# Kernel tuning notes

Measured on AMD Instinct MI355X. Metric: run time of the kernel, lower is better.

Reference implementation:

```python
import jax, jax.numpy as jnp
import numpy as np

WSZ = 8
DIM = 256
DIM_HEAD = 32
HEADS = DIM // DIM_HEAD
INNER = HEADS * DIM_HEAD
D4 = DIM // 4
SCALE = DIM_HEAD ** -0.5
EPS = 1e-5


def _rel_pos_tables():
    s = WSZ
    pos = np.stack(np.meshgrid(np.arange(s), np.arange(s), indexing='ij'), 0).reshape(2, -1).T  # (s*s, 2)
    rel = pos[:, None] - pos[None, :]
    rel[..., 0] += s - 1
    rel[..., 1] += s - 1
    idx = rel[..., 0] * (2 * s - 1) + rel[..., 1]  # (s*s, s*s)
    grid = np.stack(np.meshgrid(np.arange(-s, s + 1), np.arange(-s, s + 1), indexing='ij'), 0).reshape(2, -1).T
    return idx.astype(np.int32), grid.astype(np.float32)  # ((2s+1)^2, 2)

_REL_IDX_NP, _REL_GRID_NP = _rel_pos_tables()


def _ln(h, gamma, beta):
    m = h.mean(-1, keepdims=True)
    v = ((h - m) ** 2).mean(-1, keepdims=True)
    return (h - m) / jnp.sqrt(v + EPS) * gamma + beta


def setup_inputs() -> dict:
    key = jax.random.key(0)
    ks = jax.random.split(key, 8)
    p = {}
    p['x'] = jax.random.normal(ks[0], (4, DIM, 256, 256), jnp.float32)
    p['g'] = jnp.ones((DIM,), jnp.float32)
    p['b'] = jnp.zeros((DIM,), jnp.float32)
    p['w_qkv'] = jax.random.normal(ks[1], (3 * INNER, DIM), jnp.float32) * 0.02
    p['w_out'] = jax.random.normal(ks[2], (DIM, INNER), jnp.float32) * 0.02
    p['b_out'] = jnp.zeros((DIM,), jnp.float32)
    p['dpb_w1'] = jax.random.normal(ks[3], (2, D4), jnp.float32) * 0.02
    p['dpb_b1'] = jnp.zeros((D4,), jnp.float32)
    p['dpb_ln1_g'] = jnp.ones((D4,), jnp.float32)
    p['dpb_ln1_b'] = jnp.zeros((D4,), jnp.float32)
    p['dpb_w2'] = jax.random.normal(ks[4], (D4, D4), jnp.float32) * 0.02
    p['dpb_b2'] = jnp.zeros((D4,), jnp.float32)
    p['dpb_ln2_g'] = jnp.ones((D4,), jnp.float32)
    p['dpb_ln2_b'] = jnp.zeros((D4,), jnp.float32)
    p['dpb_w3'] = jax.random.normal(ks[5], (D4, D4), jnp.float32) * 0.02
    p['dpb_b3'] = jnp.zeros((D4,), jnp.float32)
    p['dpb_ln3_g'] = jnp.ones((D4,), jnp.float32)
    p['dpb_ln3_b'] = jnp.zeros((D4,), jnp.float32)
    p['dpb_w4'] = jax.random.normal(ks[6], (D4, 1), jnp.float32) * 0.02
    p['dpb_b4'] = jnp.zeros((1,), jnp.float32)
    return p


def reference(x, g, b, w_qkv, w_out, b_out,
              dpb_w1, dpb_b1, dpb_ln1_g, dpb_ln1_b,
              dpb_w2, dpb_b2, dpb_ln2_g, dpb_ln2_b,
              dpb_w3, dpb_b3, dpb_ln3_g, dpb_ln3_b,
              dpb_w4, dpb_b4):
    B, D, H, W = x.shape
    s = WSZ
    nH, nW = H // s, W // s
    ss = s * s

    # channel-first LayerNorm over dim axis (biased var)
    mean = x.mean(1, keepdims=True)
    var = ((x - mean) ** 2).mean(1, keepdims=True)
    xn = (x - mean) / jnp.sqrt(var + EPS) * g[None, :, None, None] + b[None, :, None, None]

    # short attention: non-overlapping windows -> (B*nH*nW, D, s, s)
    xw = xn.reshape(B, D, nH, s, nW, s).transpose(0, 2, 4, 1, 3, 5).reshape(-1, D, s, s)
    nb = xw.shape[0]

    # 1x1 conv qkv projection (no bias)
    qkv = jnp.einsum('ed,bdxy->bexy', w_qkv, xw)  # (nb, 3*INNER, s, s)
    q, k, v = jnp.split(qkv, 3, axis=1)
    def to_heads(t):  # (nb, INNER, s, s) -> (nb, heads, ss, dh)
        return t.reshape(nb, HEADS, DIM_HEAD, ss).transpose(0, 1, 3, 2)
    q, k, v = to_heads(q) * SCALE, to_heads(k), to_heads(v)

    sim = jnp.einsum('bhid,bhjd->bhij', q, k)  # (nb, heads, ss, ss)

    # dynamic position bias MLP over ((2s+1)^2, 2) relative coords
    rel = jnp.asarray(_REL_GRID_NP)
    h1 = jax.nn.relu(_ln(rel @ dpb_w1 + dpb_b1, dpb_ln1_g, dpb_ln1_b))
    h2 = jax.nn.relu(_ln(h1 @ dpb_w2 + dpb_b2, dpb_ln2_g, dpb_ln2_b))
    h3 = jax.nn.relu(_ln(h2 @ dpb_w3 + dpb_b3, dpb_ln3_g, dpb_ln3_b))
    table = (h3 @ dpb_w4 + dpb_b4)[:, 0]  # ((2s+1)^2,)
    bias = table[jnp.asarray(_REL_IDX_NP)]  # (ss, ss)

    attn = jax.nn.softmax(sim + bias, axis=-1)
    out = jnp.einsum('bhij,bhjd->bhid', attn, v)  # (nb, heads, ss, dh)
    out = out.transpose(0, 1, 3, 2).reshape(nb, INNER, s, s)

    # 1x1 conv output projection (with bias)
    out = jnp.einsum('od,bdxy->boxy', w_out, out) + b_out[None, :, None, None]

    # un-window
    out = out.reshape(B, nH, nW, D, s, s).transpose(0, 3, 1, 4, 2, 5).reshape(B, D, H, W)
    return out
```

## Files before the change

### kernel.cpp

```cpp
#include <hip/hip_runtime.h>

typedef __attribute__((ext_vector_type(8))) short short8;
typedef __attribute__((ext_vector_type(4))) float f32x4;

#define SCALE_Q 0.17677669529663687f

__device__ __forceinline__ unsigned short f2bf(float f){
  unsigned u = __builtin_bit_cast(unsigned, f);
  u = (u + 0x7FFFu + ((u >> 16) & 1u)) >> 16;
  return (unsigned short)u;
}
__device__ __forceinline__ float bf2f(unsigned short h){
  unsigned u = ((unsigned)h) << 16;
  return __builtin_bit_cast(float, u);
}

__global__ void prep_w(const float* __restrict__ w_qkv, const float* __restrict__ g,
                       const float* __restrict__ bvec, const float* __restrict__ w_out,
                       unsigned short* __restrict__ wq_b, unsigned short* __restrict__ wo_b,
                       float* __restrict__ qkvb){
  const int row  = blockIdx.x * 4 + (threadIdx.x >> 6);
  const int lane = threadIdx.x & 63;
  if (row < 768){
    const float sc = (row < 256) ? SCALE_Q : 1.0f;
    float4 w  = ((const float4*)(w_qkv + (size_t)row * 256))[lane];
    float4 gv = ((const float4*)g)[lane];
    float4 bv = ((const float4*)bvec)[lane];
    unsigned long long pk =
        (unsigned long long)f2bf(w.x * gv.x * sc)
      | ((unsigned long long)f2bf(w.y * gv.y * sc) << 16)
      | ((unsigned long long)f2bf(w.z * gv.z * sc) << 32)
      | ((unsigned long long)f2bf(w.w * gv.w * sc) << 48);
    *(unsigned long long*)(wq_b + (size_t)row * 256 + lane * 4) = pk;
    float acc = w.x * bv.x + w.y * bv.y + w.z * bv.z + w.w * bv.w;
    #pragma unroll
    for (int off = 32; off; off >>= 1) acc += __shfl_xor(acc, off);
    if (lane == 0) qkvb[row] = acc * sc;
  } else {
    const int o = row - 768;
    float4 w = ((const float4*)(w_out + (size_t)o * 256))[lane];
    unsigned long long pk =
        (unsigned long long)f2bf(w.x)
      | ((unsigned long long)f2bf(w.y) << 16)
      | ((unsigned long long)f2bf(w.z) << 32)
      | ((unsigned long long)f2bf(w.w) << 48);
    *(unsigned long long*)(wo_b + (size_t)o * 256 + lane * 4) = pk;
  }
}

__device__ __forceinline__ float wsum(float v){
  #pragma unroll
  for (int off = 32; off; off >>= 1) v += __shfl_xor(v, off);
  return v;
}
__device__ __forceinline__ float lnrelu(float h, float gamma, float beta){
  float m = wsum(h) * (1.0f / 64.0f);
  float d = h - m;
  float v = wsum(d * d) * (1.0f / 64.0f);
  float r = d * rsqrtf(v + 1e-5f) * gamma + beta;
  return fmaxf(r, 0.0f);
}
__device__ __forceinline__ float matmul64(float h, const float* __restrict__ w, int f){
  float acc = 0.0f;
  for (int k = 0; k < 64; ++k) acc += __shfl(h, k) * w[k * 64 + f];
  return acc;
}

__global__ void dpb_kernel(const float* __restrict__ w1, const float* __restrict__ b1,
                           const float* __restrict__ g1, const float* __restrict__ e1,
                           const float* __restrict__ w2, const float* __restrict__ b2,
                           const float* __restrict__ g2, const float* __restrict__ e2,
                           const float* __restrict__ w3, const float* __restrict__ b3,
                           const float* __restrict__ g3, const float* __restrict__ e3,
                           const float* __restrict__ w4, const float* __restrict__ b4,
                           float* __restrict__ table){
  const int r = blockIdx.x, f = threadIdx.x;
  const float cy = (float)(r / 17 - 8), cx = (float)(r % 17 - 8);
  float h = cy * w1[f] + cx * w1[64 + f] + b1[f];
  h = lnrelu(h, g1[f], e1[f]);
  float h2 = matmul64(h, w2, f) + b2[f];
  h2 = lnrelu(h2, g2[f], e2[f]);
  float h3 = matmul64(h2, w3, f) + b3[f];
  h3 = lnrelu(h3, g3[f], e3[f]);
  float o = wsum(h3 * w4[f]);
  if (f == 0) table[r] = o + b4[0];
}

__global__ void bias_expand(const float* __restrict__ table, float* __restrict__ bias64){
  const int id = blockIdx.x * 256 + threadIdx.x;
  const int i = id >> 6, j = id & 63;
  const int r0 = (i >> 3) - (j >> 3) + 7;
  const int r1 = (i & 7) - (j & 7) + 7;
  bias64[id] = table[r0 * 15 + r1];
}

#define LDS_TOTAL 148480

__global__ __launch_bounds__(256, 1) void attn_main(
    const float* __restrict__ x,
    const unsigned short* __restrict__ wq_b,
    const unsigned short* __restrict__ wo_b,
    const float* __restrict__ qkvb,
    const float* __restrict__ b_out,
    const float* __restrict__ bias64,
    float* __restrict__ out)
{
  extern __shared__ char smem[];
  unsigned short* xn = (unsigned short*)smem;
  unsigned short* Qs = (unsigned short*)(smem + 36864);
  unsigned short* Ks = (unsigned short*)(smem + 70656);
  unsigned short* Vt = (unsigned short*)(smem + 104448);

  const int tid = threadIdx.x, lane = tid & 63, wv = tid >> 6;
  const int blk = ((blockIdx.x & 7) << 9) | (blockIdx.x >> 3);
  const int b = blk >> 10, hb = (blk >> 5) & 31, wb = blk & 31;

  {
    const int p = lane, prow = p >> 3, pcol = p & 7;
    const float* xp = x + ((size_t)b << 24) + (size_t)(hb * 8 + prow) * 256 + (size_t)(wb * 8 + pcol);
    float sum = 0.0f, ss = 0.0f;
    unsigned short* xrow = xn + p * 264;
    #pragma unroll 8
    for (int dk = 0; dk < 64; ++dk){
      const int d = (wv << 6) + dk;
      float v = xp[(size_t)d << 16];
      sum += v; ss += v * v;
      xrow[d] = f2bf(v);
    }
    float* red = (float*)(smem + 141312);
    red[wv * 64 + p] = sum;
    red[256 + wv * 64 + p] = ss;
    __syncthreads();
    float s0 = red[p] + red[64 + p] + red[128 + p] + red[192 + p];
    float s1 = red[256 + p] + red[320 + p] + red[384 + p] + red[448 + p];
    float mean = s0 * (1.0f / 256.0f);
    float var  = s1 * (1.0f / 256.0f) - mean * mean;
    float rstd = rsqrtf(var + 1e-5f);
    if (wv == 0){ red[512 + p] = mean; red[576 + p] = rstd; }
    __syncthreads();
    const int pp = tid >> 2, qq = tid & 3;
    const float mn = red[512 + pp], rs = red[576 + pp];
    unsigned short* rowp = xn + pp * 264 + qq * 64;
    #pragma unroll
    for (int i = 0; i < 8; ++i){
      short8 v8 = *(short8*)(rowp + i * 8);
      #pragma unroll
      for (int e = 0; e < 8; ++e){
        float f = bf2f((unsigned short)v8[e]);
        v8[e] = (short)f2bf((f - mn) * rs);
      }
      *(short8*)(rowp + i * 8) = v8;
    }
  }
  __syncthreads();

  {
    const int l15 = lane & 15, l4 = lane >> 4;
    for (int c = 0; c < 3; ++c){
      const int n0 = wv * 192 + c * 64;
      f32x4 acc[4][4];
      #pragma unroll
      for (int mt = 0; mt < 4; ++mt)
        #pragma unroll
        for (int nt = 0; nt < 4; ++nt)
          acc[mt][nt] = (f32x4){0.f, 0.f, 0.f, 0.f};
      const unsigned short* bp = wq_b + (size_t)(n0 + l15) * 256 + 8 * l4;
      short8 bcur[4], bnxt[4];
      #pragma unroll
      for (int nt = 0; nt < 4; ++nt) bcur[nt] = *(const short8*)(bp + nt * 4096);
      #pragma unroll
      for (int kt = 0; kt < 8; ++kt){
        if (kt < 7){
          #pragma unroll
          for (int nt = 0; nt < 4; ++nt) bnxt[nt] = *(const short8*)(bp + nt * 4096 + (kt + 1) * 32);
        }
        short8 a[4];
        #pragma unroll
        for (int mt = 0; mt < 4; ++mt)
          a[mt] = *(const short8*)(xn + (mt * 16 + l15) * 264 + kt * 32 + 8 * l4);
        #pragma unroll
        for (int mt = 0; mt < 4; ++mt)
          #pragma unroll
          for (int nt = 0; nt < 4; ++nt)
            acc[mt][nt] = __builtin_amdgcn_mfma_f32_16x16x32_bf16(a[mt], bcur[nt], acc[mt][nt], 0, 0, 0);
        if (kt < 7){
          #pragma unroll
          for (int nt = 0; nt < 4; ++nt) bcur[nt] = bnxt[nt];
        }
      }
      const bool isV = (n0 >= 512);
      const bool isQ = (n0 < 256);
      #pragma unroll
      for (int nt = 0; nt < 4; ++nt){
        const int e = n0 + nt * 16 + l15;
        const float bv = qkvb[e];
        #pragma unroll
        for (int mt = 0; mt < 4; ++mt){
          if (!isV){
            unsigned short* dst = isQ ? Qs : Ks;
            const int col = e & 255;
            #pragma unroll
            for (int j = 0; j < 4; ++j){
              const int row = mt * 16 + (l4 << 2) + j;
              dst[row * 264 + col] = f2bf(acc[mt][nt][j] + bv);
            }
          } else {
            const int vd = e - 512;
            const int r0 = mt * 16 + (l4 << 2);
            unsigned long long pk =
                (unsigned long long)f2bf(acc[mt][nt][0] + bv)
              | ((unsigned long long)f2bf(acc[mt][nt][1] + bv) << 16)
              | ((unsigned long long)f2bf(acc[mt][nt][2] + bv) << 32)
              | ((unsigned long long)f2bf(acc[mt][nt][3] + bv) << 48);
            *(unsigned long long*)(Vt + vd * 72 + r0) = pk;
          }
        }
      }
    }
  }
  __syncthreads();

  {
    const int l15 = lane & 15, l4 = lane >> 4;
    unsigned short* Pw = ((unsigned short*)smem) + wv * 4608;
    f32x4 oacc[2][4][2];
    #pragma unroll
    for (int hh = 0; hh < 2; ++hh){
      const int h = (wv << 1) + hh;
      short8 qa[4], kb[4];
      #pragma unroll
      for (int t = 0; t < 4; ++t){
        qa[t] = *(const short8*)(Qs + (t * 16 + l15) * 264 + h * 32 + 8 * l4);
        kb[t] = *(const short8*)(Ks + (t * 16 + l15) * 264 + h * 32 + 8 * l4);
      }
      #pragma unroll
      for (int mt = 0; mt < 4; ++mt){
        f32x4 srow[4];
        #pragma unroll
        for (int nt = 0; nt < 4; ++nt){
          f32x4 z = {0.f, 0.f, 0.f, 0.f};
          srow[nt] = __builtin_amdgcn_mfma_f32_16x16x32_bf16(qa[mt], kb[nt], z, 0, 0, 0);
        }
        #pragma unroll
        for (int j = 0; j < 4; ++j){
          const int row = mt * 16 + (l4 << 2) + j;
          float v0 = srow[0][j] + bias64[row * 64 +      l15];
          float v1 = srow[1][j] + bias64[row * 64 + 16 + l15];
          float v2 = srow[2][j] + bias64[row * 64 + 32 + l15];
          float v3 = srow[3][j] + bias64[row * 64 + 48 + l15];
          float m = fmaxf(fmaxf(v0, v1), fmaxf(v2, v3));
          m = fmaxf(m, __shfl_xor(m, 1)); m = fmaxf(m, __shfl_xor(m, 2));
          m = fmaxf(m, __shfl_xor(m, 4)); m = fmaxf(m, __shfl_xor(m, 8));
          v0 = __expf(v0 - m); v1 = __expf(v1 - m);
          v2 = __expf(v2 - m); v3 = __expf(v3 - m);
          float sm = v0 + v1 + v2 + v3;
          sm += __shfl_xor(sm, 1); sm += __shfl_xor(sm, 2);
          sm += __shfl_xor(sm, 4); sm += __shfl_xor(sm, 8);
          const float inv = 1.0f / sm;
          Pw[row * 72 +      l15] = f2bf(v0 * inv);
          Pw[row * 72 + 16 + l15] = f2bf(v1 * inv);
          Pw[row * 72 + 32 + l15] = f2bf(v2 * inv);
          Pw[row * 72 + 48 + l15] = f2bf(v3 * inv);
        }
      }
      #pragma unroll
      for (int mt = 0; mt < 4; ++mt)
        #pragma unroll
        for (int nt = 0; nt < 2; ++nt)
          oacc[hh][mt][nt] = (f32x4){0.f, 0.f, 0.f, 0.f};
      #pragma unroll
      for (int kt = 0; kt < 2; ++kt){
        short8 pa[4], vb[2];
        #pragma unroll
        for (int mt = 0; mt < 4; ++mt)
          pa[mt] = *(const short8*)(Pw + (mt * 16 + l15) * 72 + kt * 32 + 8 * l4);
        #pragma unroll
        for (int nt = 0; nt < 2; ++nt)
          vb[nt] = *(const short8*)(Vt + (h * 32 + nt * 16 + l15) * 72 + kt * 32 + 8 * l4);
        #pragma unroll
        for (int mt = 0; mt < 4; ++mt)
          #pragma unroll
          for (int nt = 0; nt < 2; ++nt)
            oacc[hh][mt][nt] = __builtin_amdgcn_mfma_f32_16x16x32_bf16(pa[mt], vb[nt], oacc[hh][mt][nt], 0, 0, 0);
      }
    }
    __syncthreads();
    unsigned short* ao = (unsigned short*)smem;
    #pragma unroll
    for (int hh = 0; hh < 2; ++hh){
      const int h = (wv << 1) + hh;
      #pragma unroll
      for (int mt = 0; mt < 4; ++mt)
        #pragma unroll
        for (int nt = 0; nt < 2; ++nt)
          #pragma unroll
          for (int j = 0; j < 4; ++j)
            ao[(mt * 16 + (l4 << 2) + j) * 264 + h * 32 + nt * 16 + l15] = f2bf(oacc[hh][mt][nt][j]);
    }
  }
  __syncthreads();

  {
    const int l15 = lane & 15, l4 = lane >> 4;
    const unsigned short* ao = (const unsigned short*)smem;
    float* sw = (float*)(smem + 143872) + wv * 288;
    const int n0w = wv * 64;
    f32x4 acc[4][4];
    #pragma unroll
    for (int mt = 0; mt < 4; ++mt)
      #pragma unroll
      for (int nt = 0; nt < 4; ++nt)
        acc[mt][nt] = (f32x4){0.f, 0.f, 0.f, 0.f};
    const unsigned short* bp = wo_b + (size_t)(n0w + l15) * 256 + 8 * l4;
    short8 bcur[4], bnxt[4];
    #pragma unroll
    for (int nt = 0; nt < 4; ++nt) bcur[nt] = *(const short8*)(bp + nt * 4096);
    #pragma unroll
    for (int kt = 0; kt < 8; ++kt){
      if (kt < 7){
        #pragma unroll
        for (int nt = 0; nt < 4; ++nt) bnxt[nt] = *(const short8*)(bp + nt * 4096 + (kt + 1) * 32);
      }
      short8 a[4];
      #pragma unroll
      for (int mt = 0; mt < 4; ++mt)
        a[mt] = *(const short8*)(ao + (mt * 16 + l15) * 264 + kt * 32 + 8 * l4);
      #pragma unroll
      for (int mt = 0; mt < 4; ++mt)
        #pragma unroll
        for (int nt = 0; nt < 4; ++nt)
          acc[mt][nt] = __builtin_amdgcn_mfma_f32_16x16x32_bf16(a[mt], bcur[nt], acc[mt][nt], 0, 0, 0);
      if (kt < 7){
        #pragma unroll
        for (int nt = 0; nt < 4; ++nt) bcur[nt] = bnxt[nt];
      }
    }
    float* op = out + ((size_t)b << 24) + (size_t)(hb * 8) * 256 + (size_t)(wb * 8);
    #pragma unroll
    for (int nt = 0; nt < 4; ++nt){
      const int ebase = n0w + nt * 16;
      const float bo = b_out[ebase + l15];
      #pragma unroll
      for (int mt = 0; mt < 4; ++mt){
        #pragma unroll
        for (int j = 0; j < 4; ++j)
          sw[((l4 << 2) + j) * 17 + l15] = acc[mt][nt][j] + bo;
        asm volatile("s_waitcnt lgkmcnt(0)" ::: "memory");
        #pragma unroll
        for (int q = 0; q < 4; ++q){
          const int el = q * 4 + l4;
          float v = sw[l15 * 17 + el];
          const int p = mt * 16 + l15;
          op[(size_t)(ebase + el) * 65536 + (size_t)(p >> 3) * 256 + (p & 7)] = v;
        }
        asm volatile("s_waitcnt lgkmcnt(0)" ::: "memory");
      }
    }
  }
}

extern "C" void kernel_launch(void* const* d_in, const int* in_sizes, int n_in,
                              void* d_out, int out_size, void* d_ws, size_t ws_size,
                              hipStream_t stream){
  const float* x     = (const float*)d_in[0];
  const float* g     = (const float*)d_in[1];
  const float* bvec  = (const float*)d_in[2];
  const float* w_qkv = (const float*)d_in[3];
  const float* w_out = (const float*)d_in[4];
  const float* b_out = (const float*)d_in[5];
  float* out = (float*)d_out;

  char* ws = (char*)d_ws;
  unsigned short* wq_b  = (unsigned short*)(ws);
  unsigned short* wo_b  = (unsigned short*)(ws + 393216);
  float* qkvb   = (float*)(ws + 524288);
  float* table  = (float*)(ws + 527360);
  float* bias64 = (float*)(ws + 528640);

  prep_w<<<dim3(256), dim3(256), 0, stream>>>(w_qkv, g, bvec, w_out, wq_b, wo_b, qkvb);
  dpb_kernel<<<dim3(289), dim3(64), 0, stream>>>(
      (const float*)d_in[6],  (const float*)d_in[7],  (const float*)d_in[8],  (const float*)d_in[9],
      (const float*)d_in[10], (const float*)d_in[11], (const float*)d_in[12], (const float*)d_in[13],
      (const float*)d_in[14], (const float*)d_in[15], (const float*)d_in[16], (const float*)d_in[17],
      (const float*)d_in[18], (const float*)d_in[19], table);
  bias_expand<<<dim3(16), dim3(256), 0, stream>>>(table, bias64);

  hipFuncSetAttribute((const void*)attn_main, hipFuncAttributeMaxDynamicSharedMemorySize, LDS_TOTAL);
  attn_main<<<dim3(4096), dim3(256), LDS_TOTAL, stream>>>(x, wq_b, wo_b, qkvb, b_out, bias64, out);
}
```

Before: 1.075 ms.

## Use 1024-thread blocks with pre-tiled MFMA weights and swizzled P buffer

The main attention kernel goes from 4 to 16 waves per block. Each wave now takes a smaller slice of the QKV GEMM, one head-half of the attention, and a 32x32 tile of the output projection. The weights are pre-arranged into the MFMA fragment layout, so each lane does one contiguous 16-byte load. The softmax probability buffer uses an XOR swizzle to cut LDS bank conflicts. The aim is more latency hiding inside each CU, since only one block fits per CU because of LDS. The cost is fewer MFMAs per wave to amortise loads over, plus extra barriers.

```diff
diff --git a/kernel.cpp b/kernel.cpp
--- a/kernel.cpp
+++ b/kernel.cpp
@@ -15,37 +15,42 @@
   return __builtin_bit_cast(float, u);
 }
 
-__global__ void prep_w(const float* __restrict__ w_qkv, const float* __restrict__ g,
-                       const float* __restrict__ bvec, const float* __restrict__ w_out,
-                       unsigned short* __restrict__ wq_b, unsigned short* __restrict__ wo_b,
-                       float* __restrict__ qkvb){
-  const int row  = blockIdx.x * 4 + (threadIdx.x >> 6);
+__global__ void prep_tiled(const float* __restrict__ w_qkv, const float* __restrict__ g,
+                           const float* __restrict__ w_out,
+                           unsigned short* __restrict__ wq_t, unsigned short* __restrict__ wo_t){
+  int id = blockIdx.x * 256 + threadIdx.x;
+  const bool isQKV = (id < 24576);
+  int e, sub;
+  const float* src;
+  unsigned short* dst;
+  float sc;
+  if (isQKV){ e = id >> 5; sub = id & 31; src = w_qkv; dst = wq_t; sc = (e < 256) ? SCALE_Q : 1.0f; }
+  else { int id2 = id - 24576; e = id2 >> 5; sub = id2 & 31; src = w_out; dst = wo_t; sc = 1.0f; }
+  const int kt = sub >> 2, l4c = sub & 3;
+  const int k0 = kt * 32 + l4c * 8;
+  const int tile = e >> 4, l15c = e & 15;
+  const float4 w0 = *(const float4*)(src + (size_t)e * 256 + k0);
+  const float4 w1 = *(const float4*)(src + (size_t)e * 256 + k0 + 4);
+  float4 g0 = make_float4(1.f,1.f,1.f,1.f), g1 = g0;
+  if (isQKV){ g0 = *(const float4*)(g + k0); g1 = *(const float4*)(g + k0 + 4); }
+  short8 o;
+  o[0] = (short)f2bf(w0.x * g0.x * sc); o[1] = (short)f2bf(w0.y * g0.y * sc);
+  o[2] = (short)f2bf(w0.z * g0.z * sc); o[3] = (short)f2bf(w0.w * g0.w * sc);
+  o[4] = (short)f2bf(w1.x * g1.x * sc); o[5] = (short)f2bf(w1.y * g1.y * sc);
+  o[6] = (short)f2bf(w1.z * g1.z * sc); o[7] = (short)f2bf(w1.w * g1.w * sc);
+  *(short8*)(dst + ((size_t)(tile * 8 + kt) * 64 + (l4c * 16 + l15c)) * 8) = o;
+}
+
+__global__ void qkvb_kernel(const float* __restrict__ w_qkv, const float* __restrict__ bvec,
+                            float* __restrict__ qkvb){
+  const int row = blockIdx.x * 4 + (threadIdx.x >> 6);
   const int lane = threadIdx.x & 63;
-  if (row < 768){
-    const float sc = (row < 256) ? SCALE_Q : 1.0f;
-    float4 w  = ((const float4*)(w_qkv + (size_t)row * 256))[lane];
-    float4 gv = ((const float4*)g)[lane];
-    float4 bv = ((const float4*)bvec)[lane];
-    unsigned long long pk =
-        (unsigned long long)f2bf(w.x * gv.x * sc)
-      | ((unsigned long long)f2bf(w.y * gv.y * sc) << 16)
-      | ((unsigned long long)f2bf(w.z * gv.z * sc) << 32)
-      | ((unsigned long long)f2bf(w.w * gv.w * sc) << 48);
-    *(unsigned long long*)(wq_b + (size_t)row * 256 + lane * 4) = pk;
-    float acc = w.x * bv.x + w.y * bv.y + w.z * bv.z + w.w * bv.w;
-    #pragma unroll
-    for (int off = 32; off; off >>= 1) acc += __shfl_xor(acc, off);
-    if (lane == 0) qkvb[row] = acc * sc;
-  } else {
-    const int o = row - 768;
-    float4 w = ((const float4*)(w_out + (size_t)o * 256))[lane];
-    unsigned long long pk =
-        (unsigned long long)f2bf(w.x)
-      | ((unsigned long long)f2bf(w.y) << 16)
-      | ((unsigned long long)f2bf(w.z) << 32)
-      | ((unsigned long long)f2bf(w.w) << 48);
-    *(unsigned long long*)(wo_b + (size_t)o * 256 + lane * 4) = pk;
-  }
+  float4 w  = ((const float4*)(w_qkv + (size_t)row * 256))[lane];
+  float4 bv = ((const float4*)bvec)[lane];
+  float acc = w.x * bv.x + w.y * bv.y + w.z * bv.z + w.w * bv.w;
+  #pragma unroll
+  for (int off = 32; off; off >>= 1) acc += __shfl_xor(acc, off);
+  if (lane == 0) qkvb[row] = acc * ((row < 256) ? SCALE_Q : 1.0f);
 }
 
 __device__ __forceinline__ float wsum(float v){
@@ -94,12 +99,16 @@
   bias64[id] = table[r0 * 15 + r1];
 }
 
-#define LDS_TOTAL 148480
-
-__global__ __launch_bounds__(256, 1) void attn_main(
+#define LDS_TOTAL 146944
+
+__device__ __forceinline__ int pswz(int row, int col){
+  return row * 64 + (((col >> 3) ^ (row & 7)) << 3) + (col & 7);
+}
+
+__global__ __launch_bounds__(1024, 1) void attn_main(
     const float* __restrict__ x,
-    const unsigned short* __restrict__ wq_b,
-    const unsigned short* __restrict__ wo_b,
+    const unsigned short* __restrict__ wq_t,
+    const unsigned short* __restrict__ wo_t,
     const float* __restrict__ qkvb,
     const float* __restrict__ b_out,
     const float* __restrict__ bias64,
@@ -107,11 +116,13 @@
 {
   extern __shared__ char smem[];
   unsigned short* xn = (unsigned short*)smem;
-  unsigned short* Qs = (unsigned short*)(smem + 36864);
-  unsigned short* Ks = (unsigned short*)(smem + 70656);
-  unsigned short* Vt = (unsigned short*)(smem + 104448);
+  unsigned short* Qs = (unsigned short*)(smem + 33792);
+  unsigned short* Ks = (unsigned short*)(smem + 67584);
+  unsigned short* Vt = (unsigned short*)(smem + 101376);
+  float* red = (float*)(smem + 138240);
 
   const int tid = threadIdx.x, lane = tid & 63, wv = tid >> 6;
+  const int l15 = lane & 15, l4 = lane >> 4;
   const int blk = ((blockIdx.x & 7) << 9) | (blockIdx.x >> 3);
   const int b = blk >> 10, hb = (blk >> 5) & 31, wb = blk & 31;
 
@@ -120,29 +131,31 @@
     const float* xp = x + ((size_t)b << 24) + (size_t)(hb * 8 + prow) * 256 + (size_t)(wb * 8 + pcol);
     float sum = 0.0f, ss = 0.0f;
     unsigned short* xrow = xn + p * 264;
-    #pragma unroll 8
-    for (int dk = 0; dk < 64; ++dk){
-      const int d = (wv << 6) + dk;
+    #pragma unroll
+    for (int i = 0; i < 16; ++i){
+      const int d = (wv << 4) + i;
       float v = xp[(size_t)d << 16];
       sum += v; ss += v * v;
       xrow[d] = f2bf(v);
     }
-    float* red = (float*)(smem + 141312);
     red[wv * 64 + p] = sum;
-    red[256 + wv * 64 + p] = ss;
+    red[1024 + wv * 64 + p] = ss;
     __syncthreads();
-    float s0 = red[p] + red[64 + p] + red[128 + p] + red[192 + p];
-    float s1 = red[256 + p] + red[320 + p] + red[384 + p] + red[448 + p];
-    float mean = s0 * (1.0f / 256.0f);
-    float var  = s1 * (1.0f / 256.0f) - mean * mean;
-    float rstd = rsqrtf(var + 1e-5f);
-    if (wv == 0){ red[512 + p] = mean; red[576 + p] = rstd; }
+    if (wv == 0){
+      float s0 = 0.f, s1 = 0.f;
+      #pragma unroll
+      for (int w = 0; w < 16; ++w){ s0 += red[w * 64 + lane]; s1 += red[1024 + w * 64 + lane]; }
+      float mean = s0 * (1.0f / 256.0f);
+      float var  = s1 * (1.0f / 256.0f) - mean * mean;
+      red[2048 + lane] = mean;
+      red[2112 + lane] = rsqrtf(var + 1e-5f);
+    }
     __syncthreads();
-    const int pp = tid >> 2, qq = tid & 3;
-    const float mn = red[512 + pp], rs = red[576 + pp];
-    unsigned short* rowp = xn + pp * 264 + qq * 64;
-    #pragma unroll
-    for (int i = 0; i < 8; ++i){
+    const int pp = tid >> 4, qq = tid & 15;
+    const float mn = red[2048 + pp], rs = red[2112 + pp];
+    unsigned short* rowp = xn + pp * 264 + qq * 16;
+    #pragma unroll
+    for (int i = 0; i < 2; ++i){
       short8 v8 = *(short8*)(rowp + i * 8);
       #pragma unroll
       for (int e = 0; e < 8; ++e){
@@ -155,65 +168,48 @@
   __syncthreads();
 
   {
-    const int l15 = lane & 15, l4 = lane >> 4;
-    for (int c = 0; c < 3; ++c){
-      const int n0 = wv * 192 + c * 64;
-      f32x4 acc[4][4];
-      #pragma unroll
-      for (int mt = 0; mt < 4; ++mt)
-        #pragma unroll
-        for (int nt = 0; nt < 4; ++nt)
-          acc[mt][nt] = (f32x4){0.f, 0.f, 0.f, 0.f};
-      const unsigned short* bp = wq_b + (size_t)(n0 + l15) * 256 + 8 * l4;
-      short8 bcur[4], bnxt[4];
-      #pragma unroll
-      for (int nt = 0; nt < 4; ++nt) bcur[nt] = *(const short8*)(bp + nt * 4096);
-      #pragma unroll
-      for (int kt = 0; kt < 8; ++kt){
-        if (kt < 7){
+    const int wm = wv >> 3, wn = wv & 7;
+    f32x4 acc[2][6];
+    #pragma unroll
+    for (int mt = 0; mt < 2; ++mt)
+      #pragma unroll
+      for (int nt = 0; nt < 6; ++nt)
+        acc[mt][nt] = (f32x4){0.f, 0.f, 0.f, 0.f};
+    #pragma unroll
+    for (int kt = 0; kt < 8; ++kt){
+      short8 a0 = *(const short8*)(xn + (wm * 32 +      l15) * 264 + kt * 32 + l4 * 8);
+      short8 a1 = *(const short8*)(xn + (wm * 32 + 16 + l15) * 264 + kt * 32 + l4 * 8);
+      const unsigned short* wp = wq_t + ((size_t)(wn * 6 * 8 + kt) * 64 + lane) * 8;
+      short8 bb[6];
+      #pragma unroll
+      for (int nt = 0; nt < 6; ++nt) bb[nt] = *(const short8*)(wp + (size_t)nt * 4096);
+      #pragma unroll
+      for (int nt = 0; nt < 6; ++nt){
+        acc[0][nt] = __builtin_amdgcn_mfma_f32_16x16x32_bf16(a0, bb[nt], acc[0][nt], 0, 0, 0);
+        acc[1][nt] = __builtin_amdgcn_mfma_f32_16x16x32_bf16(a1, bb[nt], acc[1][nt], 0, 0, 0);
+      }
+    }
+    #pragma unroll
+    for (int nt = 0; nt < 6; ++nt){
+      const int e = wn * 96 + nt * 16 + l15;
+      const float bv = qkvb[e];
+      #pragma unroll
+      for (int mt = 0; mt < 2; ++mt){
+        const int r0 = wm * 32 + mt * 16 + (l4 << 2);
+        if (e < 512){
+          unsigned short* dst = (e < 256) ? Qs : Ks;
+          const int col = e & 255;
           #pragma unroll
-          for (int nt = 0; nt < 4; ++nt) bnxt[nt] = *(const short8*)(bp + nt * 4096 + (kt + 1) * 32);
-        }
-        short8 a[4];
-        #pragma unroll
-        for (int mt = 0; mt < 4; ++mt)
-          a[mt] = *(const short8*)(xn + (mt * 16 + l15) * 264 + kt * 32 + 8 * l4);
-        #pragma unroll
-        for (int mt = 0; mt < 4; ++mt)
-          #pragma unroll
-          for (int nt = 0; nt < 4; ++nt)
-            acc[mt][nt] = __builtin_amdgcn_mfma_f32_16x16x32_bf16(a[mt], bcur[nt], acc[mt][nt], 0, 0, 0);
-        if (kt < 7){
-          #pragma unroll
-          for (int nt = 0; nt < 4; ++nt) bcur[nt] = bnxt[nt];
-        }
-      }
-      const bool isV = (n0 >= 512);
-      const bool isQ = (n0 < 256);
-      #pragma unroll
-      for (int nt = 0; nt < 4; ++nt){
-        const int e = n0 + nt * 16 + l15;
-        const float bv = qkvb[e];
-        #pragma unroll
-        for (int mt = 0; mt < 4; ++mt){
-          if (!isV){
-            unsigned short* dst = isQ ? Qs : Ks;
-            const int col = e & 255;
-            #pragma unroll
-            for (int j = 0; j < 4; ++j){
-              const int row = mt * 16 + (l4 << 2) + j;
-              dst[row * 264 + col] = f2bf(acc[mt][nt][j] + bv);
-            }
-          } else {
-            const int vd = e - 512;
-            const int r0 = mt * 16 + (l4 << 2);
-            unsigned long long pk =
-                (unsigned long long)f2bf(acc[mt][nt][0] + bv)
-              | ((unsigned long long)f2bf(acc[mt][nt][1] + bv) << 16)
-              | ((unsigned long long)f2bf(acc[mt][nt][2] + bv) << 32)
-              | ((unsigned long long)f2bf(acc[mt][nt][3] + bv) << 48);
-            *(unsigned long long*)(Vt + vd * 72 + r0) = pk;
-          }
+          for (int j = 0; j < 4; ++j)
+            dst[(r0 + j) * 264 + col] = f2bf(acc[mt][nt][j] + bv);
+        } else {
+          const int vd = e - 512;
+          unsigned long long pk =
+              (unsigned long long)f2bf(acc[mt][nt][0] + bv)
+            | ((unsigned long long)f2bf(acc[mt][nt][1] + bv) << 16)
+            | ((unsigned long long)f2bf(acc[mt][nt][2] + bv) << 32)
+            | ((unsigned long long)f2bf(acc[mt][nt][3] + bv) << 48);
+          *(unsigned long long*)(Vt + vd * 72 + r0) = pk;
         }
       }
     }
@@ -221,136 +217,120 @@
   __syncthreads();
 
   {
-    const int l15 = lane & 15, l4 = lane >> 4;
-    unsigned short* Pw = ((unsigned short*)smem) + wv * 4608;
-    f32x4 oacc[2][4][2];
-    #pragma unroll
-    for (int hh = 0; hh < 2; ++hh){
-      const int h = (wv << 1) + hh;
-      short8 qa[4], kb[4];
-      #pragma unroll
-      for (int t = 0; t < 4; ++t){
-        qa[t] = *(const short8*)(Qs + (t * 16 + l15) * 264 + h * 32 + 8 * l4);
-        kb[t] = *(const short8*)(Ks + (t * 16 + l15) * 264 + h * 32 + 8 * l4);
-      }
-      #pragma unroll
-      for (int mt = 0; mt < 4; ++mt){
-        f32x4 srow[4];
-        #pragma unroll
-        for (int nt = 0; nt < 4; ++nt){
-          f32x4 z = {0.f, 0.f, 0.f, 0.f};
-          srow[nt] = __builtin_amdgcn_mfma_f32_16x16x32_bf16(qa[mt], kb[nt], z, 0, 0, 0);
-        }
-        #pragma unroll
-        for (int j = 0; j < 4; ++j){
-          const int row = mt * 16 + (l4 << 2) + j;
-          float v0 = srow[0][j] + bias64[row * 64 +      l15];
-          float v1 = srow[1][j] + bias64[row * 64 + 16 + l15];
-          float v2 = srow[2][j] + bias64[row * 64 + 32 + l15];
-          float v3 = srow[3][j] + bias64[row * 64 + 48 + l15];
-          float m = fmaxf(fmaxf(v0, v1), fmaxf(v2, v3));
-          m = fmaxf(m, __shfl_xor(m, 1)); m = fmaxf(m, __shfl_xor(m, 2));
-          m = fmaxf(m, __shfl_xor(m, 4)); m = fmaxf(m, __shfl_xor(m, 8));
-          v0 = __expf(v0 - m); v1 = __expf(v1 - m);
-          v2 = __expf(v2 - m); v3 = __expf(v3 - m);
-          float sm = v0 + v1 + v2 + v3;
-          sm += __shfl_xor(sm, 1); sm += __shfl_xor(sm, 2);
-          sm += __shfl_xor(sm, 4); sm += __shfl_xor(sm, 8);
-          const float inv = 1.0f / sm;
-          Pw[row * 72 +      l15] = f2bf(v0 * inv);
-          Pw[row * 72 + 16 + l15] = f2bf(v1 * inv);
-          Pw[row * 72 + 32 + l15] = f2bf(v2 * inv);
-          Pw[row * 72 + 48 + l15] = f2bf(v3 * inv);
-        }
-      }
-      #pragma unroll
-      for (int mt = 0; mt < 4; ++mt)
+    const int h = wv >> 1, half = wv & 1;
+    short8 qa[2], kb[4];
+    #pragma unroll
+    for (int mt = 0; mt < 2; ++mt)
+      qa[mt] = *(const short8*)(Qs + (half * 32 + mt * 16 + l15) * 264 + h * 32 + l4 * 8);
+    #pragma unroll
+    for (int t = 0; t < 4; ++t)
+      kb[t] = *(const short8*)(Ks + (t * 16 + l15) * 264 + h * 32 + l4 * 8);
+    __syncthreads();
+
+    unsigned short* Pw = (unsigned short*)smem + h * 4096;
+    #pragma unroll
+    for (int mt = 0; mt < 2; ++mt){
+      f32x4 srow[4];
+      #pragma unroll
+      for (int nt = 0; nt < 4; ++nt){
+        f32x4 z = {0.f, 0.f, 0.f, 0.f};
+        srow[nt] = __builtin_amdgcn_mfma_f32_16x16x32_bf16(qa[mt], kb[nt], z, 0, 0, 0);
+      }
+      #pragma unroll
+      for (int j = 0; j < 4; ++j){
+        const int row = half * 32 + mt * 16 + (l4 << 2) + j;
+        float v0 = srow[0][j] + bias64[row * 64 +      l15];
+        float v1 = srow[1][j] + bias64[row * 64 + 16 + l15];
+        float v2 = srow[2][j] + bias64[row * 64 + 32 + l15];
+        float v3 = srow[3][j] + bias64[row * 64 + 48 + l15];
+        float m = fmaxf(fmaxf(v0, v1), fmaxf(v2, v3));
+        m = fmaxf(m, __shfl_xor(m, 1)); m = fmaxf(m, __shfl_xor(m, 2));
+        m = fmaxf(m, __shfl_xor(m, 4)); m = fmaxf(m, __shfl_xor(m, 8));
+        v0 = __expf(v0 - m); v1 = __expf(v1 - m);
+        v2 = __expf(v2 - m); v3 = __expf(v3 - m);
+        float sm = v0 + v1 + v2 + v3;
+        sm += __shfl_xor(sm, 1); sm += __shfl_xor(sm, 2);
+        sm += __shfl_xor(sm, 4); sm += __shfl_xor(sm, 8);
+        const float inv = 1.0f / sm;
+        Pw[pswz(row,      l15)] = f2bf(v0 * inv);
+        Pw[pswz(row, 16 + l15)] = f2bf(v1 * inv);
+        Pw[pswz(row, 32 + l15)] = f2bf(v2 * inv);
+        Pw[pswz(row, 48 + l15)] = f2bf(v3 * inv);
+      }
+    }
+    f32x4 oacc[2][2];
+    #pragma unroll
+    for (int mt = 0; mt < 2; ++mt)
+      #pragma unroll
+      for (int nt = 0; nt < 2; ++nt)
+        oacc[mt][nt] = (f32x4){0.f, 0.f, 0.f, 0.f};
+    #pragma unroll
+    for (int ktv = 0; ktv < 2; ++ktv){
+      short8 pa[2], vb[2];
+      #pragma unroll
+      for (int mt = 0; mt < 2; ++mt){
+        const int row = half * 32 + mt * 16 + l15;
+        pa[mt] = *(const short8*)(Pw + row * 64 + (((ktv * 4 + l4) ^ (row & 7)) << 3));
+      }
+      #pragma unroll
+      for (int nt = 0; nt < 2; ++nt)
+        vb[nt] = *(const short8*)(Vt + (h * 32 + nt * 16 + l15) * 72 + ktv * 32 + l4 * 8);
+      #pragma unroll
+      for (int mt = 0; mt < 2; ++mt)
         #pragma unroll
         for (int nt = 0; nt < 2; ++nt)
-          oacc[hh][mt][nt] = (f32x4){0.f, 0.f, 0.f, 0.f};
-      #pragma unroll
-      for (int kt = 0; kt < 2; ++kt){
-        short8 pa[4], vb[2];
-        #pragma unroll
-        for (int mt = 0; mt < 4; ++mt)
-          pa[mt] = *(const short8*)(Pw + (mt * 16 + l15) * 72 + kt * 32 + 8 * l4);
-        #pragma unroll
-        for (int nt = 0; nt < 2; ++nt)
-          vb[nt] = *(const short8*)(Vt + (h * 32 + nt * 16 + l15) * 72 + kt * 32 + 8 * l4);
-        #pragma unroll
-        for (int mt = 0; mt < 4; ++mt)
-          #pragma unroll
-          for (int nt = 0; nt < 2; ++nt)
-            oacc[hh][mt][nt] = __builtin_amdgcn_mfma_f32_16x16x32_bf16(pa[mt], vb[nt], oacc[hh][mt][nt], 0, 0, 0);
-      }
+          oacc[mt][nt] = __builtin_amdgcn_mfma_f32_16x16x32_bf16(pa[mt], vb[nt], oacc[mt][nt], 0, 0, 0);
     }
     __syncthreads();
     unsigned short* ao = (unsigned short*)smem;
     #pragma unroll
-    for (int hh = 0; hh < 2; ++hh){
-      const int h = (wv << 1) + hh;
-      #pragma unroll
-      for (int mt = 0; mt < 4; ++mt)
+    for (int mt = 0; mt < 2; ++mt)
+      #pragma unroll
+      for (int nt = 0; nt < 2; ++nt)
         #pragma unroll
-        for (int nt = 0; nt < 2; ++nt)
-          #pragma unroll
-          for (int j = 0; j < 4; ++j)
-            ao[(mt * 16 + (l4 << 2) + j) * 264 + h * 32 + nt * 16 + l15] = f2bf(oacc[hh][mt][nt][j]);
-    }
+        for (int j = 0; j < 4; ++j)
+          ao[(half * 32 + mt * 16 + (l4 << 2) + j) * 264 + h * 32 + nt * 16 + l15] = f2bf(oacc[mt][nt][j]);
   }
   __syncthreads();
 
   {
-    const int l15 = lane & 15, l4 = lane >> 4;
+    const int wm = wv >> 3, wn = wv & 7;
     const unsigned short* ao = (const unsigned short*)smem;
-    float* sw = (float*)(smem + 143872) + wv * 288;
-    const int n0w = wv * 64;
-    f32x4 acc[4][4];
-    #pragma unroll
-    for (int mt = 0; mt < 4; ++mt)
-      #pragma unroll
-      for (int nt = 0; nt < 4; ++nt)
+    float* sw = (float*)(smem + 33792) + wv * 288;
+    f32x4 acc[2][2];
+    #pragma unroll
+    for (int mt = 0; mt < 2; ++mt)
+      #pragma unroll
+      for (int nt = 0; nt < 2; ++nt)
         acc[mt][nt] = (f32x4){0.f, 0.f, 0.f, 0.f};
-    const unsigned short* bp = wo_b + (size_t)(n0w + l15) * 256 + 8 * l4;
-    short8 bcur[4], bnxt[4];
-    #pragma unroll
-    for (int nt = 0; nt < 4; ++nt) bcur[nt] = *(const short8*)(bp + nt * 4096);
     #pragma unroll
     for (int kt = 0; kt < 8; ++kt){
-      if (kt < 7){
-        #pragma unroll
-        for (int nt = 0; nt < 4; ++nt) bnxt[nt] = *(const short8*)(bp + nt * 4096 + (kt + 1) * 32);
-      }
-      short8 a[4];
-      #pragma unroll
-      for (int mt = 0; mt < 4; ++mt)
-        a[mt] = *(const short8*)(ao + (mt * 16 + l15) * 264 + kt * 32 + 8 * l4);
-      #pragma unroll
-      for (int mt = 0; mt < 4; ++mt)
-        #pragma unroll
-        for (int nt = 0; nt < 4; ++nt)
-          acc[mt][nt] = __builtin_amdgcn_mfma_f32_16x16x32_bf16(a[mt], bcur[nt], acc[mt][nt], 0, 0, 0);
-      if (kt < 7){
-        #pragma unroll
-        for (int nt = 0; nt < 4; ++nt) bcur[nt] = bnxt[nt];
-      }
+      short8 a0 = *(const short8*)(ao + (wm * 32 +      l15) * 264 + kt * 32 + l4 * 8);
+      short8 a1 = *(const short8*)(ao + (wm * 32 + 16 + l15) * 264 + kt * 32 + l4 * 8);
+      const unsigned short* wp = wo_t + ((size_t)(wn * 2 * 8 + kt) * 64 + lane) * 8;
+      short8 b0 = *(const short8*)(wp);
+      short8 b1 = *(const short8*)(wp + 4096);
+      acc[0][0] = __builtin_amdgcn_mfma_f32_16x16x32_bf16(a0, b0, acc[0][0], 0, 0, 0);
+      acc[1][0] = __builtin_amdgcn_mfma_f32_16x16x32_bf16(a1, b0, acc[1][0], 0, 0, 0);
+      acc[0][1] = __builtin_amdgcn_mfma_f32_16x16x32_bf16(a0, b1, acc[0][1], 0, 0, 0);
+      acc[1][1] = __builtin_amdgcn_mfma_f32_16x16x32_bf16(a1, b1, acc[1][1], 0, 0, 0);
     }
     float* op = out + ((size_t)b << 24) + (size_t)(hb * 8) * 256 + (size_t)(wb * 8);
     #pragma unroll
-    for (int nt = 0; nt < 4; ++nt){
-      const int ebase = n0w + nt * 16;
+    for (int nt = 0; nt < 2; ++nt){
+      const int ebase = wn * 32 + nt * 16;
       const float bo = b_out[ebase + l15];
       #pragma unroll
-      for (int mt = 0; mt < 4; ++mt){
+      for (int mt = 0; mt < 2; ++mt){
         #pragma unroll
         for (int j = 0; j < 4; ++j)
-          sw[((l4 << 2) + j) * 17 + l15] = acc[mt][nt][j] + bo;
+          sw[((l4 << 2) + j) * 18 + l15] = acc[mt][nt][j] + bo;
         asm volatile("s_waitcnt lgkmcnt(0)" ::: "memory");
         #pragma unroll
         for (int q = 0; q < 4; ++q){
           const int el = q * 4 + l4;
-          float v = sw[l15 * 17 + el];
-          const int p = mt * 16 + l15;
+          float v = sw[l15 * 18 + el];
+          const int p = wm * 32 + mt * 16 + l15;
           op[(size_t)(ebase + el) * 65536 + (size_t)(p >> 3) * 256 + (p & 7)] = v;
         }
         asm volatile("s_waitcnt lgkmcnt(0)" ::: "memory");
@@ -371,13 +351,14 @@
   float* out = (float*)d_out;
 
   char* ws = (char*)d_ws;
-  unsigned short* wq_b  = (unsigned short*)(ws);
-  unsigned short* wo_b  = (unsigned short*)(ws + 393216);
+  unsigned short* wq_t  = (unsigned short*)(ws);
+  unsigned short* wo_t  = (unsigned short*)(ws + 393216);
   float* qkvb   = (float*)(ws + 524288);
   float* table  = (float*)(ws + 527360);
   float* bias64 = (float*)(ws + 528640);
 
-  prep_w<<<dim3(256), dim3(256), 0, stream>>>(w_qkv, g, bvec, w_out, wq_b, wo_b, qkvb);
+  prep_tiled<<<dim3(128), dim3(256), 0, stream>>>(w_qkv, g, w_out, wq_t, wo_t);
+  qkvb_kernel<<<dim3(192), dim3(256), 0, stream>>>(w_qkv, bvec, qkvb);
   dpb_kernel<<<dim3(289), dim3(64), 0, stream>>>(
       (const float*)d_in[6],  (const float*)d_in[7],  (const float*)d_in[8],  (const float*)d_in[9],
       (const float*)d_in[10], (const float*)d_in[11], (const float*)d_in[12], (const float*)d_in[13],
@@ -386,5 +367,5 @@
   bias_expand<<<dim3(16), dim3(256), 0, stream>>>(table, bias64);
 
   hipFuncSetAttribute((const void*)attn_main, hipFuncAttributeMaxDynamicSharedMemorySize, LDS_TOTAL);
-  attn_main<<<dim3(4096), dim3(256), LDS_TOTAL, stream>>>(x, wq_b, wo_b, qkvb, b_out, bias64, out);
-}
+  attn_main<<<dim3(4096), dim3(1024), LDS_TOTAL, stream>>>(x, wq_t, wo_t, qkvb, b_out, bias64, out);
+}
```

After: 862.2 us. -19.8%, faster.
